# Kernel tuning notes

Measured on AMD Instinct MI355X. Metric: run time of the kernel, lower is better.

The kernel has to match this reference:

```python
import jax, jax.numpy as jnp
import numpy as np
import math

B, NX, NY = 4, 64, 64
IN_DIM, OUT_DIM = 3, 3
DIM, DEPTH, HEADS, DH, FF_MULT = 192, 6, 8, 64, 4
INNER = HEADS * DH              # 512
FF = DIM * FF_MULT              # 768
M = int(DH * math.log(DH))      # 266 random features (performer default)
GROUPS = 8
LATENT_STEPS = 1
EPS_SN, EPS_K, EPS_GN = 1e-5, 1e-4, 1e-5


def setup_inputs() -> dict:
    rng = np.random.default_rng(0)
    f = lambda *s: jnp.asarray(rng.standard_normal(s).astype(np.float32) * 0.02)
    # unitary forward operator (SVD-whitened in torch == orthogonal matrix)
    Q, _ = np.linalg.qr(rng.standard_normal((DIM, DIM)).astype(np.float32))
    return {
        "x": jnp.asarray(rng.standard_normal((B, NX, NY, IN_DIM)).astype(np.float32)),
        "to_in_w": f(DIM, IN_DIM), "to_in_b": f(DIM),
        "pos_emb": f(1, NX * NY, DIM),
        "proj": jnp.asarray(rng.standard_normal((DEPTH, M, DH)).astype(np.float32)),
        "sn_attn_g": jnp.ones((DEPTH,), jnp.float32),
        "wq": f(DEPTH, INNER, DIM), "wk": f(DEPTH, INNER, DIM), "wv": f(DEPTH, INNER, DIM),
        "wo": f(DEPTH, DIM, INNER), "bo": f(DEPTH, DIM),
        "sn_ff_g": jnp.ones((DEPTH,), jnp.float32),
        "w1": f(DEPTH, FF, DIM), "b1": f(DEPTH, FF),
        "w2": f(DEPTH, DIM, FF), "b2": f(DEPTH, DIM),
        "expand_w": f(DIM, DIM),
        "fwd_w": jnp.asarray(Q.astype(np.float32)),
        "dec_lin_w": f(DIM, DIM), "dec_lin_b": f(DIM),
        "gn_g": jnp.ones((DIM,), jnp.float32), "gn_b": jnp.zeros((DIM,), jnp.float32),
        "c9_w": f(DIM, DIM // GROUPS, 9, 9), "c9_b": f(DIM),
        "c7_w": f(DIM // 2, DIM // GROUPS, 7, 7), "c7_b": f(DIM // 2),
        "c5_w": f(DIM // 4, (DIM // 2) // GROUPS, 5, 5), "c5_b": f(DIM // 4),
        "c1_w": f(OUT_DIM, DIM // 4, 1, 1), "c1_b": f(OUT_DIM),
        "latent_steps": LATENT_STEPS,
    }


def _scalenorm(x, g):
    n = jnp.linalg.norm(x, axis=-1, keepdims=True) * (x.shape[-1] ** -0.5)
    return x / jnp.maximum(n, EPS_SN) * g


def _softmax_features(data, proj, is_query):
    # data: [b,h,n,d]; proj: [m,d] -> FAVOR+ softmax-kernel features [b,h,n,m]
    dn = data.shape[-1] ** -0.25
    ratio = proj.shape[0] ** -0.5
    dd = jnp.einsum('bhnd,md->bhnm', data * dn, proj)
    diag = 0.5 * jnp.sum(data * data, -1) * (dn * dn)  # [b,h,n]
    if is_query:
        mx = jnp.max(dd, axis=-1, keepdims=True)
    else:
        mx = jnp.max(dd, axis=(-1, -2), keepdims=True)
    return ratio * (jnp.exp(dd - diag[..., None] - mx) + EPS_K)


def _attn(x, proj, wq, wk, wv, wo, bo):
    b, n, _ = x.shape
    split = lambda t: t.reshape(b, n, HEADS, DH).transpose(0, 2, 1, 3)
    q = split(x @ wq.T); k = split(x @ wk.T); v = split(x @ wv.T)
    qp = _softmax_features(q, proj, True)
    kp = _softmax_features(k, proj, False)
    context = jnp.einsum('bhnm,bhnd->bhmd', kp, v)            # [b,h,m,d]
    denom = jnp.einsum('bhnm,bhm->bhn', qp, kp.sum(2))
    out = jnp.einsum('bhnm,bhmd->bhnd', qp, context) / denom[..., None]
    out = out.transpose(0, 2, 1, 3).reshape(b, n, INNER)
    return out @ wo.T + bo


def _circ_conv(x, w, b, groups):
    p = w.shape[-1] // 2
    x = jnp.pad(x, ((0, 0), (0, 0), (p, p), (p, p)), mode='wrap')
    y = jax.lax.conv_general_dilated(x, w, (1, 1), 'VALID',
        dimension_numbers=('NCHW', 'OIHW', 'NCHW'), feature_group_count=groups)
    return y + b[None, :, None, None]


def _group_norm(x, g, b):
    B_, C, H, W = x.shape
    xg = x.reshape(B_, GROUPS, C // GROUPS, H, W)
    mu = xg.mean((2, 3, 4), keepdims=True)
    var = xg.var((2, 3, 4), keepdims=True)
    xn = ((xg - mu) * jax.lax.rsqrt(var + EPS_GN)).reshape(B_, C, H, W)
    return xn * g[None, :, None, None] + b[None, :, None, None]


def reference(x, to_in_w, to_in_b, pos_emb, proj, sn_attn_g, wq, wk, wv, wo, bo,
              sn_ff_g, w1, b1, w2, b2, expand_w, fwd_w, dec_lin_w, dec_lin_b,
              gn_g, gn_b, c9_w, c9_b, c7_w, c7_b, c5_w, c5_b, c1_w, c1_b, latent_steps):
    b, nx, ny, _ = x.shape
    h = x @ to_in_w.T + to_in_b                       # [b,nx,ny,dim]
    h = h.reshape(b, nx * ny, DIM) + pos_emb[:, :nx * ny]
    for i in range(DEPTH):                             # Performer: prenorm attn + prenorm FF
        h = h + _attn(_scalenorm(h, sn_attn_g[i]), proj[i], wq[i], wk[i], wv[i], wo[i], bo[i])
        hn = _scalenorm(h, sn_ff_g[i])
        h = h + (jax.nn.gelu(hn @ w1[i].T + b1[i], approximate=False) @ w2[i].T + b2[i])
    h = h.reshape(b, nx, ny, DIM) @ expand_w.T        # expand_latent (no bias)
    u, us = h, []
    for _ in range(latent_steps):
        u = u @ fwd_w.T                               # unitary forward operator
        us.append(u)
    u = jnp.concatenate(us, 0)                        # [(b*t), nx, ny, c]
    y = u @ dec_lin_w.T + dec_lin_b
    y = y.transpose(0, 3, 1, 2)                       # NCHW
    y = _group_norm(y, gn_g, gn_b)
    y = jax.nn.gelu(_circ_conv(y, c9_w, c9_b, GROUPS), approximate=False)
    y = jax.nn.gelu(_circ_conv(y, c7_w, c7_b, GROUPS), approximate=False)
    y = jax.nn.gelu(_circ_conv(y, c5_w, c5_b, GROUPS), approximate=False)
    y = jax.lax.conv_general_dilated(y, c1_w, (1, 1), 'VALID',
        dimension_numbers=('NCHW', 'OIHW', 'NCHW')) + c1_b[None, :, None, None]
    # einops '(b t) c nx ny -> b t nx ny c'
    y = y.reshape(b, latent_steps, OUT_DIM, nx, ny).transpose(0, 1, 3, 4, 2)
    return y
```

## Files before the change

kernel.cpp:

```cpp
#include <hip/hip_runtime.h>
#include <cmath>

#define NB      4
#define NTOK    4096
#define BNTOK   16384
#define CDIM    192
#define CINNER  512
#define NHEADS  8
#define DHEAD   64
#define CFF     768
#define MFEAT   266
#define NDEPTH  6

#define DN      0.35355339059327373f
#define RATIO   0.06131393394849658f

typedef unsigned short u16;
typedef __attribute__((ext_vector_type(8))) short s16x8;
typedef __attribute__((ext_vector_type(8))) u16  u16x8;
typedef __attribute__((ext_vector_type(4))) float f32x4;

#define OFF_H    0ull
#define OFF_HN   3145728ull
#define OFF_Q    6291456ull
#define OFF_K    14680064ull
#define OFF_V    23068672ull
#define OFF_BIG  31457280ull
#define OFF_PJ   44040192ull
#define OFF_CTXT 44163072ull
#define OFF_KMAX 47368192ull
#define OFF_GNP  47368448ull
#define OFF_GNS  47369472ull
#define OFF_WHI  47370240ull
#define OFF_WLO  49489920ull
#define WOFF_QKV 0ull
#define WOFF_WO  1769472ull
#define WOFF_W1  2359296ull
#define WOFF_W2  3244032ull
#define WOFF_EXP 4128768ull
#define WOFF_FWD 4165632ull
#define WOFF_DEC 4202496ull

#define PJL      20480
#define NSEG     16
#define CTXP     20800

__device__ __forceinline__ float gelu_f(float x) {
    return 0.5f * x * (1.0f + erff(x * 0.7071067811865476f));
}
__device__ __forceinline__ unsigned f2ord(float f) {
    int i = __float_as_int(f);
    return (i >= 0) ? ((unsigned)i | 0x80000000u) : (unsigned)(~i);
}
__device__ __forceinline__ float ord2f(unsigned u) {
    int i = (u & 0x80000000u) ? (int)(u & 0x7fffffffu) : ~(int)u;
    return __int_as_float(i);
}
__device__ __forceinline__ void split_bf16(float a, u16& h, u16& l) {
    unsigned ua = __float_as_uint(a);
    unsigned rh = (ua + 0x7FFFu + ((ua >> 16) & 1u)) >> 16;
    h = (u16)rh;
    float hf = __uint_as_float(rh << 16);
    float lo = a - hf;
    unsigned ul = __float_as_uint(lo);
    unsigned rl = (ul + 0x7FFFu + ((ul >> 16) & 1u)) >> 16;
    l = (u16)rl;
}
__device__ __forceinline__ u16 hi_bf16(float a) {
    unsigned ua = __float_as_uint(a);
    return (u16)((ua + 0x7FFFu + ((ua >> 16) & 1u)) >> 16);
}

__global__ __launch_bounds__(256) void cvt_qkv(const float* __restrict__ wq,
    const float* __restrict__ wk, const float* __restrict__ wv,
    u16* __restrict__ hi, u16* __restrict__ lo)
{
    int idx = blockIdx.x * 256 + threadIdx.x;
    int l = idx / 294912, rem = idx - l * 294912;
    int r = rem / 192, c = rem - r * 192;
    float v;
    if (r < 512)       v = wq[((size_t)l * 512 + r) * 192 + c];
    else if (r < 1024) v = wk[((size_t)l * 512 + (r - 512)) * 192 + c];
    else               v = wv[((size_t)l * 512 + (r - 1024)) * 192 + c];
    u16 h, lw; split_bf16(v, h, lw);
    hi[idx] = h; lo[idx] = lw;
}

__global__ __launch_bounds__(256) void cvt_w(const float* __restrict__ src,
    u16* __restrict__ hi, u16* __restrict__ lo, int n)
{
    int idx = blockIdx.x * 256 + threadIdx.x;
    if (idx < n) {
        u16 h, l; split_bf16(src[idx], h, l);
        hi[idx] = h; lo[idx] = l;
    }
}

__global__ __launch_bounds__(256) void cvt_dec(const float* __restrict__ e,
    const float* __restrict__ f, const float* __restrict__ d,
    u16* __restrict__ hi, u16* __restrict__ lo)
{
    int idx = blockIdx.x * 256 + threadIdx.x;
    if (idx >= 110592) return;
    int which = idx / 36864, rem = idx - which * 36864;
    float v = (which == 0) ? e[rem] : (which == 1) ? f[rem] : d[rem];
    u16 h, l; split_bf16(v, h, l);
    hi[idx] = h; lo[idx] = l;
}

__global__ __launch_bounds__(256) void cvt_pj(const float* __restrict__ proj,
    u16* __restrict__ hi, u16* __restrict__ lo)
{
    int idx = blockIdx.x * 256 + threadIdx.x;
    int l = idx / PJL, rem = idx - l * PJL;
    int m = rem >> 6, k = rem & 63;
    float v = (m < MFEAT) ? proj[(size_t)l * MFEAT * DHEAD + m * 64 + k] : 0.f;
    u16 h, lw; split_bf16(v, h, lw);
    hi[idx] = h; lo[idx] = lw;
}

__global__ __launch_bounds__(256) void input_embed(const float* __restrict__ x,
    const float* __restrict__ w, const float* __restrict__ bvec,
    const float* __restrict__ pos, float* __restrict__ h)
{
    int idx = blockIdx.x * 256 + threadIdx.x;
    int row = idx / CDIM, c = idx - row * CDIM;
    int p = row & (NTOK - 1);
    const float* xr = x + (size_t)row * 3;
    h[idx] = xr[0]*w[c*3+0] + xr[1]*w[c*3+1] + xr[2]*w[c*3+2] + bvec[c] + pos[(size_t)p*CDIM + c];
}

__global__ __launch_bounds__(256) void rownorm_kernel(const float* __restrict__ in,
    float* __restrict__ sv, const float* __restrict__ gptr, int gidx)
{
    int wv = threadIdx.x >> 6, lane = threadIdx.x & 63;
    int row = blockIdx.x * 4 + wv;
    const float* p = in + (size_t)row * CDIM;
    float x0 = p[lane], x1 = p[lane + 64], x2 = p[lane + 128];
    float ss = x0*x0 + x1*x1 + x2*x2;
    #pragma unroll
    for (int off = 32; off; off >>= 1) ss += __shfl_xor(ss, off);
    if (lane == 0) {
        float g = gptr[gidx];
        float n = sqrtf(ss * (1.0f / 192.0f));
        sv[row] = g / fmaxf(n, 1e-5f);
    }
}

#define LP 40
__global__ __launch_bounds__(256) void gemm_mfma(const float* __restrict__ A,
    const float* __restrict__ ascale,
    const u16* __restrict__ Bhi, const u16* __restrict__ Blo,
    const float* __restrict__ bias, const float* __restrict__ resid,
    float* __restrict__ C, int M, int N, int K, int epi)
{
    __shared__ u16 a_hi[128 * LP], a_lo[128 * LP], b_hi[128 * LP], b_lo[128 * LP];
    const int tid = threadIdx.x;
    const int n0 = blockIdx.x * 128, m0 = blockIdx.y * 128;
    const int wave = tid >> 6, lane = tid & 63;
    const int wr = wave >> 1, wc = wave & 1;
    const int fr = lane & 15, q = lane >> 4;
    const bool wactive = (n0 + wc * 64) < N;
    f32x4 acc[4][4];
    #pragma unroll
    for (int i = 0; i < 4; ++i)
        #pragma unroll
        for (int j = 0; j < 4; ++j) { acc[i][j][0]=0.f; acc[i][j][1]=0.f; acc[i][j][2]=0.f; acc[i][j][3]=0.f; }

    const int srow = tid >> 1, sc0 = (tid & 1) * 16;
    const float* aptr = A + (size_t)(m0 + srow) * K + sc0;
    const float as = ascale ? ascale[m0 + srow] : 1.0f;
    const bool bval = (n0 + srow) < N;
    const u16* bhp = Bhi + (size_t)(n0 + srow) * K + sc0;
    const u16* blp = Blo + (size_t)(n0 + srow) * K + sc0;
    const int soff = srow * LP + sc0;
    const int aoffb = (wr * 64 + fr) * LP + q * 8;
    const int boffb = (wc * 64 + fr) * LP + q * 8;

    for (int kc = 0; kc < K; kc += 32) {
        float4 f0 = *(const float4*)(aptr + kc);
        float4 f1 = *(const float4*)(aptr + kc + 4);
        float4 f2 = *(const float4*)(aptr + kc + 8);
        float4 f3 = *(const float4*)(aptr + kc + 12);
        u16x8 h0, l0, h1, l1;
        {
            float v[16] = {f0.x,f0.y,f0.z,f0.w, f1.x,f1.y,f1.z,f1.w,
                           f2.x,f2.y,f2.z,f2.w, f3.x,f3.y,f3.z,f3.w};
            u16 hh[16], ll[16];
            #pragma unroll
            for (int i = 0; i < 16; ++i) { float sv = v[i] * as; split_bf16(sv, hh[i], ll[i]); }
            #pragma unroll
            for (int i = 0; i < 8; ++i) { h0[i]=hh[i]; l0[i]=ll[i]; h1[i]=hh[8+i]; l1[i]=ll[8+i]; }
        }
        *(u16x8*)&a_hi[soff]     = h0;  *(u16x8*)&a_hi[soff + 8] = h1;
        *(u16x8*)&a_lo[soff]     = l0;  *(u16x8*)&a_lo[soff + 8] = l1;
        u16x8 bh0 = (u16x8)0, bh1 = (u16x8)0, bl0 = (u16x8)0, bl1 = (u16x8)0;
        if (bval) {
            bh0 = *(const u16x8*)(bhp + kc);  bh1 = *(const u16x8*)(bhp + kc + 8);
            bl0 = *(const u16x8*)(blp + kc);  bl1 = *(const u16x8*)(blp + kc + 8);
        }
        *(u16x8*)&b_hi[soff]     = bh0;  *(u16x8*)&b_hi[soff + 8] = bh1;
        *(u16x8*)&b_lo[soff]     = bl0;  *(u16x8*)&b_lo[soff + 8] = bl1;
        __syncthreads();
        if (wactive) {
            s16x8 Ah[4], Al[4], Bh[4], Bl[4];
            #pragma unroll
            for (int t = 0; t < 4; ++t) {
                Ah[t] = *(const s16x8*)&a_hi[aoffb + t * 16 * LP];
                Al[t] = *(const s16x8*)&a_lo[aoffb + t * 16 * LP];
                Bh[t] = *(const s16x8*)&b_hi[boffb + t * 16 * LP];
                Bl[t] = *(const s16x8*)&b_lo[boffb + t * 16 * LP];
            }
            #pragma unroll
            for (int i = 0; i < 4; ++i)
                #pragma unroll
                for (int j = 0; j < 4; ++j)
                    acc[i][j] = __builtin_amdgcn_mfma_f32_16x16x32_bf16(Ah[i], Bh[j], acc[i][j], 0, 0, 0);
            #pragma unroll
            for (int i = 0; i < 4; ++i)
                #pragma unroll
                for (int j = 0; j < 4; ++j)
                    acc[i][j] = __builtin_amdgcn_mfma_f32_16x16x32_bf16(Ah[i], Bl[j], acc[i][j], 0, 0, 0);
            #pragma unroll
            for (int i = 0; i < 4; ++i)
                #pragma unroll
                for (int j = 0; j < 4; ++j)
                    acc[i][j] = __builtin_amdgcn_mfma_f32_16x16x32_bf16(Al[i], Bh[j], acc[i][j], 0, 0, 0);
        }
        __syncthreads();
    }
    const int c0 = n0 + wc * 64;
    const int rowb = m0 + wr * 64;
    #pragma unroll
    for (int j = 0; j < 4; ++j) {
        int c = c0 + j * 16 + fr;
        if (c >= N) continue;
        float bb = (epi & 1) ? bias[c] : 0.f;
        float* cp;
        if (epi & 8) cp = C + (size_t)(c >> 9) * 8388608ull + (size_t)(c & 511);
        else         cp = C + c;
        const float* rp = (epi & 4) ? (resid + c) : nullptr;
        #pragma unroll
        for (int i = 0; i < 4; ++i) {
            #pragma unroll
            for (int r = 0; r < 4; ++r) {
                int row = rowb + i * 16 + q * 4 + r;
                float val = acc[i][j][r] + bb;
                if (epi & 2) val = gelu_f(val);
                if (epi & 4) val += rp[(size_t)row * N];
                size_t off = (epi & 8) ? (size_t)row * 512 : (size_t)row * N;
                cp[off] = val;
            }
        }
    }
}

__global__ void kmax_init(unsigned* kmaxu) {
    if (threadIdx.x < NDEPTH * 32) kmaxu[threadIdx.x] = 0u;
}

__global__ __launch_bounds__(256) void kmax2_kernel(const float* __restrict__ Km,
    const u16* __restrict__ pjh, unsigned* __restrict__ kmaxu)
{
    __shared__ __align__(16) u16 khi[64 * 72];
    __shared__ float wred[4];
    const int tid = threadIdx.x;
    const int nt = blockIdx.x, bh = blockIdx.y;
    const int b = bh >> 3, hh = bh & 7;
    const int wave = tid >> 6, lane = tid & 63;
    const int fr = lane & 15, quad = lane >> 4;
    float lm = -1e30f;
    const size_t kbase = ((size_t)b * NTOK) * CINNER + hh * DHEAD;
    for (int ch = 0; ch < 4; ++ch) {
        const int n0 = nt * 256 + ch * 64;
        __syncthreads();
        {
            int tok = tid >> 2, koff = (tid & 3) * 16;
            const float* kp = Km + kbase + (size_t)(n0 + tok) * CINNER + koff;
            u16 hh16[16];
            #pragma unroll
            for (int qd = 0; qd < 4; ++qd) {
                float4 f = *(const float4*)(kp + qd * 4);
                hh16[qd*4+0] = hi_bf16(f.x * DN); hh16[qd*4+1] = hi_bf16(f.y * DN);
                hh16[qd*4+2] = hi_bf16(f.z * DN); hh16[qd*4+3] = hi_bf16(f.w * DN);
            }
            u16x8 v0, v1;
            #pragma unroll
            for (int i = 0; i < 8; ++i) { v0[i] = hh16[i]; v1[i] = hh16[8+i]; }
            *(u16x8*)&khi[tok * 72 + koff] = v0;
            *(u16x8*)&khi[tok * 72 + koff + 8] = v1;
        }
        __syncthreads();
        int rowA = (wave * 16 + fr) * 72;
        s16x8 A0 = *(const s16x8*)&khi[rowA + quad * 8];
        s16x8 A1 = *(const s16x8*)&khi[rowA + 32 + quad * 8];
        for (int ct = 0; ct < 17; ++ct) {
            const u16* bp = pjh + (ct * 16 + fr) * 64 + quad * 8;
            s16x8 B0 = *(const s16x8*)bp;
            s16x8 B1 = *(const s16x8*)(bp + 32);
            f32x4 t; t[0]=0.f; t[1]=0.f; t[2]=0.f; t[3]=0.f;
            t = __builtin_amdgcn_mfma_f32_16x16x32_bf16(A0, B0, t, 0, 0, 0);
            t = __builtin_amdgcn_mfma_f32_16x16x32_bf16(A1, B1, t, 0, 0, 0);
            if (ct * 16 + fr < MFEAT) {
                #pragma unroll
                for (int r = 0; r < 4; ++r) lm = fmaxf(lm, t[r]);
            }
        }
    }
    #pragma unroll
    for (int off = 32; off; off >>= 1) lm = fmaxf(lm, __shfl_xor(lm, off));
    if (lane == 0) wred[wave] = lm;
    __syncthreads();
    if (tid == 0) {
        float m = fmaxf(fmaxf(wred[0], wred[1]), fmaxf(wred[2], wred[3]));
        atomicMax(kmaxu + bh, f2ord(m));
    }
}

__global__ __launch_bounds__(256) void ctx2_kernel(const float* __restrict__ Km,
    const float* __restrict__ Vm, const u16* __restrict__ pjh, const u16* __restrict__ pjl,
    const unsigned* __restrict__ kmaxu, float* __restrict__ part)
{
    __shared__ __align__(16) u16 khi[32 * 72], klo[32 * 72];
    __shared__ __align__(16) u16 vth[80 * 40], vtl[80 * 40];
    __shared__ __align__(16) u16 kph[4][16 * 40], kpl[4][16 * 40];
    __shared__ float diag[32];
    const int tid = threadIdx.x;
    const int bh = blockIdx.x, seg = blockIdx.y;
    const int b = bh >> 3, hh = bh & 7;
    const int wave = tid >> 6, lane = tid & 63;
    const int fr = lane & 15, quad = lane >> 4;
    const float kmx = ord2f(kmaxu[bh]);
    for (int i = tid; i < 16 * 40; i += 256) {
        int row = 64 + i / 40, col = i - (i / 40) * 40;
        vth[row * 40 + col] = (row == 64) ? (u16)0x3F80 : (u16)0;
        vtl[row * 40 + col] = 0;
    }
    f32x4 accv[5][5];
    #pragma unroll
    for (int i = 0; i < 5; ++i)
        #pragma unroll
        for (int j = 0; j < 5; ++j) { accv[i][j][0]=0.f; accv[i][j][1]=0.f; accv[i][j][2]=0.f; accv[i][j][3]=0.f; }
    const size_t rowbase = ((size_t)b * NTOK) * CINNER + hh * DHEAD;
    u16* sh = kph[wave];  u16* sl = kpl[wave];
    for (int nc = 0; nc < 8; ++nc) {
        const int n0 = seg * 256 + nc * 32;
        __syncthreads();
        {
            int tok = tid >> 3, koff = (tid & 7) * 8;
            const float* kp = Km + rowbase + (size_t)(n0 + tok) * CINNER + koff;
            float4 f0 = *(const float4*)kp;
            float4 f1 = *(const float4*)(kp + 4);
            float v[8] = {f0.x*DN, f0.y*DN, f0.z*DN, f0.w*DN, f1.x*DN, f1.y*DN, f1.z*DN, f1.w*DN};
            u16x8 hv, lv; float ps = 0.f;
            #pragma unroll
            for (int i = 0; i < 8; ++i) { u16 h, l; split_bf16(v[i], h, l); hv[i]=h; lv[i]=l; ps += v[i]*v[i]; }
            *(u16x8*)&khi[tok * 72 + koff] = hv;
            *(u16x8*)&klo[tok * 72 + koff] = lv;
            ps += __shfl_xor(ps, 1); ps += __shfl_xor(ps, 2); ps += __shfl_xor(ps, 4);
            if ((tid & 7) == 0) diag[tok] = 0.5f * ps;
            const float* vp = Vm + rowbase + (size_t)(n0 + tok) * CINNER + koff;
            float4 g0 = *(const float4*)vp;
            float4 g1 = *(const float4*)(vp + 4);
            float vv[8] = {g0.x, g0.y, g0.z, g0.w, g1.x, g1.y, g1.z, g1.w};
            #pragma unroll
            for (int i = 0; i < 8; ++i) {
                u16 h, l; split_bf16(vv[i], h, l);
                vth[(koff + i) * 40 + tok] = h;
                vtl[(koff + i) * 40 + tok] = l;
            }
        }
        __syncthreads();
        s16x8 Ah[2][2], Al[2][2];
        #pragma unroll
        for (int rt = 0; rt < 2; ++rt) {
            int rowA = (rt * 16 + fr) * 72;
            Ah[rt][0] = *(const s16x8*)&khi[rowA + quad * 8];
            Ah[rt][1] = *(const s16x8*)&khi[rowA + 32 + quad * 8];
            Al[rt][0] = *(const s16x8*)&klo[rowA + quad * 8];
            Al[rt][1] = *(const s16x8*)&klo[rowA + 32 + quad * 8];
        }
        for (int mc = 0; mc < 5; ++mc) {
            const int ct = mc * 4 + wave;
            const u16* bph = pjh + (ct * 16 + fr) * 64 + quad * 8;
            const u16* bpl = pjl + (ct * 16 + fr) * 64 + quad * 8;
            s16x8 B0h = *(const s16x8*)bph, B1h = *(const s16x8*)(bph + 32);
            s16x8 B0l = *(const s16x8*)bpl, B1l = *(const s16x8*)(bpl + 32);
            const bool valid = (ct * 16 + fr) < MFEAT;
            #pragma unroll
            for (int rt = 0; rt < 2; ++rt) {
                f32x4 dd; dd[0]=0.f; dd[1]=0.f; dd[2]=0.f; dd[3]=0.f;
                dd = __builtin_amdgcn_mfma_f32_16x16x32_bf16(Ah[rt][0], B0h, dd, 0, 0, 0);
                dd = __builtin_amdgcn_mfma_f32_16x16x32_bf16(Ah[rt][0], B0l, dd, 0, 0, 0);
                dd = __builtin_amdgcn_mfma_f32_16x16x32_bf16(Al[rt][0], B0h, dd, 0, 0, 0);
                dd = __builtin_amdgcn_mfma_f32_16x16x32_bf16(Ah[rt][1], B1h, dd, 0, 0, 0);
                dd = __builtin_amdgcn_mfma_f32_16x16x32_bf16(Ah[rt][1], B1l, dd, 0, 0, 0);
                dd = __builtin_amdgcn_mfma_f32_16x16x32_bf16(Al[rt][1], B1h, dd, 0, 0, 0);
                ushort4 ph, pl;
                #pragma unroll
                for (int r = 0; r < 4; ++r) {
                    float dgv = diag[rt * 16 + quad * 4 + r];
                    float val = valid ? RATIO * (expf(dd[r] - dgv - kmx) + 1e-4f) : 0.f;
                    u16 h, l; split_bf16(val, h, l);
                    (&ph.x)[r] = h; (&pl.x)[r] = l;
                }
                *(ushort4*)&sh[fr * 40 + rt * 16 + quad * 4] = ph;
                *(ushort4*)&sl[fr * 40 + rt * 16 + quad * 4] = pl;
            }
            s16x8 Bh = *(const s16x8*)&sh[fr * 40 + quad * 8];
            s16x8 Bl = *(const s16x8*)&sl[fr * 40 + quad * 8];
            #pragma unroll
            for (int rt2 = 0; rt2 < 5; ++rt2) {
                s16x8 Vh = *(const s16x8*)&vth[(rt2 * 16 + fr) * 40 + quad * 8];
                s16x8 Vl = *(const s16x8*)&vtl[(rt2 * 16 + fr) * 40 + quad * 8];
                accv[rt2][mc] = __builtin_amdgcn_mfma_f32_16x16x32_bf16(Vh, Bh, accv[rt2][mc], 0, 0, 0);
                accv[rt2][mc] = __builtin_amdgcn_mfma_f32_16x16x32_bf16(Vh, Bl, accv[rt2][mc], 0, 0, 0);
                accv[rt2][mc] = __builtin_amdgcn_mfma_f32_16x16x32_bf16(Vl, Bh, accv[rt2][mc], 0, 0, 0);
            }
        }
    }
    float* pb = part + ((size_t)(seg * 32 + bh)) * CTXP;
    #pragma unroll
    for (int rt2 = 0; rt2 < 5; ++rt2) {
        #pragma unroll
        for (int mc = 0; mc < 5; ++mc) {
            int ct = mc * 4 + wave;
            #pragma unroll
            for (int r = 0; r < 4; ++r) {
                int row = rt2 * 16 + quad * 4 + r;
                if (row < 65)
                    pb[(size_t)row * 320 + ct * 16 + fr] = accv[rt2][mc][r];
            }
        }
    }
}

__global__ __launch_bounds__(256) void ctxt_reduce(const float* __restrict__ part,
    u16* __restrict__ cth, u16* __restrict__ ctl)
{
    int idx = blockIdx.x * 256 + threadIdx.x;
    if (idx >= 32 * CTXP) return;
    float s = 0.f;
    #pragma unroll
    for (int sg = 0; sg < NSEG; ++sg) s += part[(size_t)sg * 32 * CTXP + idx];
    int bh = idx / CTXP, rem = idx - bh * CTXP;
    int row = rem / 320, col = rem - row * 320;
    u16 h, l; split_bf16(s, h, l);
    size_t o = ((size_t)bh * 80 + row) * 320 + col;
    cth[o] = h; ctl[o] = l;
}

__global__ __launch_bounds__(256) void qside2_kernel(const float* __restrict__ Qm,
    const u16* __restrict__ pjh, const u16* __restrict__ pjl,
    const u16* __restrict__ cth, const u16* __restrict__ ctl,
    float* __restrict__ attn_out)
{
    __shared__ __align__(16) u16 qhi[64 * 72], qlo[64 * 72];
    __shared__ __align__(16) u16 slabh[4][16 * 72], slabl[4][16 * 72];
    __shared__ float diag[64];
    const int tid = threadIdx.x;
    const int nt = blockIdx.x, bh = blockIdx.y;
    const int b = bh >> 3, hh = bh & 7;
    const int wave = tid >> 6, lane = tid & 63;
    const int fr = lane & 15, quad = lane >> 4;
    const int n0 = nt * 64;
    {
        int tok = tid >> 2, koff = (tid & 3) * 16;
        const float* qp = Qm + ((size_t)(b * NTOK + n0 + tok)) * CINNER + hh * DHEAD + koff;
        float v[16]; float ps = 0.f;
        #pragma unroll
        for (int qd = 0; qd < 4; ++qd) {
            float4 f = *(const float4*)(qp + qd * 4);
            v[qd*4+0]=f.x*DN; v[qd*4+1]=f.y*DN; v[qd*4+2]=f.z*DN; v[qd*4+3]=f.w*DN;
        }
        u16x8 h0, l0, h1, l1;
        #pragma unroll
        for (int i = 0; i < 8; ++i) {
            u16 h, l; split_bf16(v[i], h, l); h0[i]=h; l0[i]=l;
            split_bf16(v[8+i], h, l); h1[i]=h; l1[i]=l;
        }
        #pragma unroll
        for (int i = 0; i < 16; ++i) ps += v[i]*v[i];
        *(u16x8*)&qhi[tok * 72 + koff] = h0;  *(u16x8*)&qhi[tok * 72 + koff + 8] = h1;
        *(u16x8*)&qlo[tok * 72 + koff] = l0;  *(u16x8*)&qlo[tok * 72 + koff + 8] = l1;
        ps += __shfl_xor(ps, 1); ps += __shfl_xor(ps, 2);
        if ((tid & 3) == 0) diag[tok] = 0.5f * ps;
    }
    __syncthreads();
    f32x4 dd[20];
    #pragma unroll
    for (int ct = 0; ct < 20; ++ct) { dd[ct][0]=0.f; dd[ct][1]=0.f; dd[ct][2]=0.f; dd[ct][3]=0.f; }
    {
        int rowA = (wave * 16 + fr) * 72;
        s16x8 A0h = *(const s16x8*)&qhi[rowA + quad * 8];
        s16x8 A1h = *(const s16x8*)&qhi[rowA + 32 + quad * 8];
        s16x8 A0l = *(const s16x8*)&qlo[rowA + quad * 8];
        s16x8 A1l = *(const s16x8*)&qlo[rowA + 32 + quad * 8];
        #pragma unroll
        for (int ct = 0; ct < 20; ++ct) {
            const u16* bph = pjh + (ct * 16 + fr) * 64 + quad * 8;
            const u16* bpl = pjl + (ct * 16 + fr) * 64 + quad * 8;
            s16x8 B0h = *(const s16x8*)bph, B1h = *(const s16x8*)(bph + 32);
            s16x8 B0l = *(const s16x8*)bpl, B1l = *(const s16x8*)(bpl + 32);
            dd[ct] = __builtin_amdgcn_mfma_f32_16x16x32_bf16(A0h, B0h, dd[ct], 0, 0, 0);
            dd[ct] = __builtin_amdgcn_mfma_f32_16x16x32_bf16(A0h, B0l, dd[ct], 0, 0, 0);
            dd[ct] = __builtin_amdgcn_mfma_f32_16x16x32_bf16(A0l, B0h, dd[ct], 0, 0, 0);
            dd[ct] = __builtin_amdgcn_mfma_f32_16x16x32_bf16(A1h, B1h, dd[ct], 0, 0, 0);
            dd[ct] = __builtin_amdgcn_mfma_f32_16x16x32_bf16(A1h, B1l, dd[ct], 0, 0, 0);
            dd[ct] = __builtin_amdgcn_mfma_f32_16x16x32_bf16(A1l, B1h, dd[ct], 0, 0, 0);
        }
    }
    float pm[4] = {-1e30f, -1e30f, -1e30f, -1e30f};
    #pragma unroll
    for (int ct = 0; ct < 20; ++ct) {
        if (ct * 16 + fr < MFEAT) {
            #pragma unroll
            for (int r = 0; r < 4; ++r) pm[r] = fmaxf(pm[r], dd[ct][r]);
        }
    }
    #pragma unroll
    for (int r = 0; r < 4; ++r) {
        pm[r] = fmaxf(pm[r], __shfl_xor(pm[r], 1));
        pm[r] = fmaxf(pm[r], __shfl_xor(pm[r], 2));
        pm[r] = fmaxf(pm[r], __shfl_xor(pm[r], 4));
        pm[r] = fmaxf(pm[r], __shfl_xor(pm[r], 8));
    }
    float dg[4];
    #pragma unroll
    for (int r = 0; r < 4; ++r) dg[r] = diag[wave * 16 + quad * 4 + r];
    #pragma unroll
    for (int ct = 0; ct < 20; ++ct) {
        bool valid = (ct * 16 + fr) < MFEAT;
        #pragma unroll
        for (int r = 0; r < 4; ++r)
            dd[ct][r] = valid ? RATIO * (expf(dd[ct][r] - dg[r] - pm[r]) + 1e-4f) : 0.f;
    }
    f32x4 acc[5];
    #pragma unroll
    for (int dt = 0; dt < 5; ++dt) { acc[dt][0]=0.f; acc[dt][1]=0.f; acc[dt][2]=0.f; acc[dt][3]=0.f; }
    u16* sh = slabh[wave];  u16* sl = slabl[wave];
    for (int mc = 0; mc < 5; ++mc) {
        #pragma unroll
        for (int c = 0; c < 4; ++c) {
            int ct = mc * 4 + c;
            #pragma unroll
            for (int r = 0; r < 4; ++r) {
                u16 h, l; split_bf16(dd[ct][r], h, l);
                int tok = quad * 4 + r;
                sh[tok * 72 + c * 16 + fr] = h;
                sl[tok * 72 + c * 16 + fr] = l;
            }
        }
        #pragma unroll
        for (int ks = 0; ks < 2; ++ks) {
            s16x8 Ah = *(const s16x8*)&sh[fr * 72 + ks * 32 + quad * 8];
            s16x8 Al = *(const s16x8*)&sl[fr * 72 + ks * 32 + quad * 8];
            #pragma unroll
            for (int dt = 0; dt < 5; ++dt) {
                const u16* bph = cth + ((size_t)bh * 80 + dt * 16 + fr) * 320 + mc * 64 + ks * 32 + quad * 8;
                const u16* bpl = ctl + ((size_t)bh * 80 + dt * 16 + fr) * 320 + mc * 64 + ks * 32 + quad * 8;
                s16x8 Bh = *(const s16x8*)bph;
                s16x8 Bl = *(const s16x8*)bpl;
                acc[dt] = __builtin_amdgcn_mfma_f32_16x16x32_bf16(Ah, Bh, acc[dt], 0, 0, 0);
                acc[dt] = __builtin_amdgcn_mfma_f32_16x16x32_bf16(Ah, Bl, acc[dt], 0, 0, 0);
                acc[dt] = __builtin_amdgcn_mfma_f32_16x16x32_bf16(Al, Bh, acc[dt], 0, 0, 0);
            }
        }
    }
    #pragma unroll
    for (int r = 0; r < 4; ++r) {
        float denom = __shfl(acc[4][r], lane & 48);
        float inv = 1.0f / denom;
        int token = n0 + wave * 16 + quad * 4 + r;
        float* op = attn_out + ((size_t)(b * NTOK + token)) * CINNER + hh * DHEAD;
        #pragma unroll
        for (int dt = 0; dt < 4; ++dt)
            op[dt * 16 + fr] = acc[dt][r] * inv;
    }
}

__global__ __launch_bounds__(256) void gn_part_kernel(const float* __restrict__ y,
    float2* __restrict__ part)
{
    __shared__ float s_s[256], s_q[256];
    const int tid = threadIdx.x;
    const int sp = blockIdx.x, g = blockIdx.y, b = blockIdx.z;
    int p = sp * 256 + tid;
    const float* base = y + ((size_t)(b * NTOK + p)) * CDIM + g * 24;
    float s = 0.f, q = 0.f;
    #pragma unroll
    for (int i = 0; i < 24; ++i) { float v = base[i]; s += v; q += v * v; }
    s_s[tid] = s; s_q[tid] = q;
    __syncthreads();
    for (int st = 128; st; st >>= 1) {
        if (tid < st) { s_s[tid] += s_s[tid + st]; s_q[tid] += s_q[tid + st]; }
        __syncthreads();
    }
    if (tid == 0) part[(b * 8 + g) * 16 + sp] = make_float2(s_s[0], s_q[0]);
}

__global__ void gn_stat_kernel(const float2* __restrict__ part, float2* __restrict__ stat)
{
    int bg = threadIdx.x;
    if (bg < 32) {
        float s = 0.f, q = 0.f;
        for (int i = 0; i < 16; ++i) { float2 v = part[bg * 16 + i]; s += v.x; q += v.y; }
        float mean = s * (1.0f / 98304.0f);
        float var = q * (1.0f / 98304.0f) - mean * mean;
        stat[bg] = make_float2(mean, rsqrtf(var + 1e-5f));
    }
}

__global__ __launch_bounds__(256) void gn_apply_kernel(const float* __restrict__ y,
    const float2* __restrict__ stat, const float* __restrict__ gg,
    const float* __restrict__ gb, float* __restrict__ out)
{
    __shared__ float tile[64][65];
    const int tid = threadIdx.x;
    const int pt = blockIdx.x, ct = blockIdx.y, b = blockIdx.z;
    const int p0 = pt * 64, c0 = ct * 64;
    #pragma unroll
    for (int r = 0; r < 4; ++r) {
        int id = tid + r * 256;
        int pr = id >> 4, kq = (id & 15) * 4;
        float4 v = *(const float4*)(y + ((size_t)(b * NTOK + p0 + pr)) * CDIM + c0 + kq);
        tile[pr][kq+0] = v.x; tile[pr][kq+1] = v.y; tile[pr][kq+2] = v.z; tile[pr][kq+3] = v.w;
    }
    __syncthreads();
    const int cc = tid >> 6, pp = tid & 63;
    #pragma unroll
    for (int i = 0; i < 16; ++i) {
        int c = c0 + cc * 16 + i;
        int g = c / 24;
        float2 st = stat[b * 8 + g];
        float v = tile[pp][cc * 16 + i];
        out[((size_t)(b * CDIM + c)) * NTOK + p0 + pp] = (v - st.x) * st.y * gg[c] + gb[c];
    }
}

template<int KS, int CIN, int COUT, int OX, int YS, int OCB>
__global__ __launch_bounds__(256) void circ_conv4(const float* __restrict__ in,
    const float* __restrict__ w, const float* __restrict__ bias,
    float* __restrict__ out, int do_gelu)
{
    constexpr int P   = KS / 2;
    constexpr int ICG = CIN / 8;
    constexpr int OCG = COUT / 8;
    constexpr int TW  = 64 + 2 * P;
    constexpr int TR  = 64 / YS + 2 * P;
    constexpr int RS0 = (TW + 3) & ~3;
    constexpr int RS  = (RS0 % 8 == 0) ? RS0 + 4 : RS0;
    constexpr int TCX = 64 / OX;
    constexpr int RV  = (OX + KS - 1 + 3) & ~3;
    constexpr int NLD = (TR * TW + 255) / 256;
    __shared__ __align__(16) float tile[2][TR * RS];
    const int tid = threadIdx.x;
    const int oc0 = blockIdx.x * OCB;
    const int y0  = blockIdx.y * (64 / YS);
    const int b   = blockIdx.z;
    const int g   = oc0 / OCG;
    const int tx  = tid % TCX, ty = tid / TCX;
    int srcs[NLD], dsts[NLD];
    #pragma unroll
    for (int j = 0; j < NLD; ++j) {
        int idx = tid + j * 256;
        if (idx < TR * TW) {
            int r = idx / TW, c = idx - r * TW;
            int gy = (y0 + r - P) & 63, gx = (c - P) & 63;
            srcs[j] = gy * 64 + gx;
            dsts[j] = r * RS + c;
        } else { srcs[j] = 0; dsts[j] = -1; }
    }
    float acc[OCB][OX] = {};
    const float* ip0 = in + ((size_t)(b * CIN + g * ICG)) * 4096;
    #pragma unroll 1
    for (int ic = 0; ic < ICG; ic += 2) {
        __syncthreads();
        const float* ipa = ip0 + (size_t)ic * 4096;
        const float* ipb = ipa + 4096;
        #pragma unroll
        for (int j = 0; j < NLD; ++j)
            if (dsts[j] >= 0) {
                tile[0][dsts[j]] = ipa[srcs[j]];
                tile[1][dsts[j]] = ipb[srcs[j]];
            }
        __syncthreads();
        #pragma unroll 1
        for (int pp = 0; pp < 2; ++pp) {
            const float* wp = w + ((size_t)oc0 * ICG + ic + pp) * (KS * KS);
            const float* tp = tile[pp];
            #pragma unroll 1
            for (int ky = 0; ky < KS; ++ky) {
                float wreg[OCB][KS];
                #pragma unroll
                for (int oc = 0; oc < OCB; ++oc)
                    #pragma unroll
                    for (int kx = 0; kx < KS; ++kx)
                        wreg[oc][kx] = wp[(size_t)oc * ICG * KS * KS + ky * KS + kx];
                float rv[RV];
                const float* rp = &tp[(ty + ky) * RS + tx * OX];
                #pragma unroll
                for (int q2 = 0; q2 < RV / 4; ++q2)
                    *(float4*)&rv[q2 * 4] = *(const float4*)(rp + q2 * 4);
                #pragma unroll
                for (int kx = 0; kx < KS; ++kx)
                    #pragma unroll
                    for (int oc = 0; oc < OCB; ++oc)
                        #pragma unroll
                        for (int ox = 0; ox < OX; ++ox)
                            acc[oc][ox] += rv[kx + ox] * wreg[oc][kx];
            }
        }
    }
    const int y = y0 + ty, x = tx * OX;
    #pragma unroll
    for (int oc = 0; oc < OCB; ++oc) {
        float bv = bias[oc0 + oc];
        float vo[OX];
        #pragma unroll
        for (int ox = 0; ox < OX; ++ox) {
            float vv = acc[oc][ox] + bv;
            vo[ox] = do_gelu ? gelu_f(vv) : vv;
        }
        float* op = out + (((size_t)(b * COUT + oc0 + oc) * 64 + y)) * 64 + x;
        #pragma unroll
        for (int q2 = 0; q2 < OX / 4; ++q2)
            *(float4*)(op + q2 * 4) = *(float4*)&vo[q2 * 4];
    }
}

__global__ __launch_bounds__(256) void conv1_kernel(const float* __restrict__ in,
    const float* __restrict__ w, const float* __restrict__ bias, float* __restrict__ out)
{
    int idx = blockIdx.x * 256 + threadIdx.x;
    int b = idx >> 12, p = idx & 4095;
    float a0 = bias[0], a1 = bias[1], a2 = bias[2];
    const float* ip = in + (size_t)b * 48 * NTOK + p;
    #pragma unroll 8
    for (int ic = 0; ic < 48; ++ic) {
        float v = ip[(size_t)ic * NTOK];
        a0 += v * w[ic]; a1 += v * w[48 + ic]; a2 += v * w[96 + ic];
    }
    float* op = out + (size_t)idx * 3;
    op[0] = a0; op[1] = a1; op[2] = a2;
}

static inline void gemm_mf(hipStream_t s, const float* A, const float* ascale,
                           const u16* Bhi, const u16* Blo,
                           const float* bias, const float* resid, float* C,
                           int M, int N, int K, int epi)
{
    dim3 g((N + 127) / 128, M / 128);
    hipLaunchKernelGGL(gemm_mfma, g, dim3(256), 0, s, A, ascale, Bhi, Blo, bias, resid, C, M, N, K, epi);
}

extern "C" void kernel_launch(void* const* d_in, const int* in_sizes, int n_in,
                              void* d_out, int out_size, void* d_ws, size_t ws_size,
                              hipStream_t stream)
{
    (void)in_sizes; (void)n_in; (void)out_size; (void)ws_size;
    const float* x        = (const float*)d_in[0];
    const float* to_in_w  = (const float*)d_in[1];
    const float* to_in_b  = (const float*)d_in[2];
    const float* pos_emb  = (const float*)d_in[3];
    const float* proj     = (const float*)d_in[4];
    const float* sn_attn_g= (const float*)d_in[5];
    const float* wq       = (const float*)d_in[6];
    const float* wk       = (const float*)d_in[7];
    const float* wv       = (const float*)d_in[8];
    const float* wo       = (const float*)d_in[9];
    const float* bo       = (const float*)d_in[10];
    const float* sn_ff_g  = (const float*)d_in[11];
    const float* w1       = (const float*)d_in[12];
    const float* b1       = (const float*)d_in[13];
    const float* w2       = (const float*)d_in[14];
    const float* b2       = (const float*)d_in[15];
    const float* expand_w = (const float*)d_in[16];
    const float* fwd_w    = (const float*)d_in[17];
    const float* dec_lin_w= (const float*)d_in[18];
    const float* dec_lin_b= (const float*)d_in[19];
    const float* gn_g     = (const float*)d_in[20];
    const float* gn_b     = (const float*)d_in[21];
    const float* c9_w     = (const float*)d_in[22];
    const float* c9_b     = (const float*)d_in[23];
    const float* c7_w     = (const float*)d_in[24];
    const float* c7_b     = (const float*)d_in[25];
    const float* c5_w     = (const float*)d_in[26];
    const float* c5_b     = (const float*)d_in[27];
    const float* c1_w     = (const float*)d_in[28];
    const float* c1_b     = (const float*)d_in[29];
    float* out = (float*)d_out;

    float* ws = (float*)d_ws;
    float* h   = ws + OFF_H;
    float* hn  = ws + OFF_HN;
    float* sbuf = ws + OFF_HN;
    float* q   = ws + OFF_Q;
    float* k   = ws + OFF_K;
    float* v   = ws + OFF_V;
    float* big = ws + OFF_BIG;
    u16* pjhi = (u16*)(ws + OFF_PJ);
    u16* pjlo = pjhi + 6 * PJL;
    u16* cthi = (u16*)(ws + OFF_CTXT);
    u16* ctlo = cthi + 32 * 80 * 320;
    unsigned* kmaxu = (unsigned*)(ws + OFF_KMAX);
    float2* gnp = (float2*)(ws + OFF_GNP);
    float2* gns = (float2*)(ws + OFF_GNS);
    u16* whi = (u16*)(ws + OFF_WHI);
    u16* wlo = (u16*)(ws + OFF_WLO);

    hipLaunchKernelGGL(input_embed, dim3(BNTOK * CDIM / 256), dim3(256), 0, stream,
                       x, to_in_w, to_in_b, pos_emb, h);
    hipLaunchKernelGGL(kmax_init, dim3(1), dim3(256), 0, stream, kmaxu);
    hipLaunchKernelGGL(cvt_qkv, dim3(6912), dim3(256), 0, stream, wq, wk, wv,
                       whi + WOFF_QKV, wlo + WOFF_QKV);
    hipLaunchKernelGGL(cvt_w, dim3(2304), dim3(256), 0, stream, wo, whi + WOFF_WO, wlo + WOFF_WO, 589824);
    hipLaunchKernelGGL(cvt_w, dim3(3456), dim3(256), 0, stream, w1, whi + WOFF_W1, wlo + WOFF_W1, 884736);
    hipLaunchKernelGGL(cvt_w, dim3(3456), dim3(256), 0, stream, w2, whi + WOFF_W2, wlo + WOFF_W2, 884736);
    hipLaunchKernelGGL(cvt_dec, dim3(432), dim3(256), 0, stream, expand_w, fwd_w, dec_lin_w,
                       whi + WOFF_EXP, wlo + WOFF_EXP);
    hipLaunchKernelGGL(cvt_pj, dim3(480), dim3(256), 0, stream, proj, pjhi, pjlo);

    for (int l = 0; l < NDEPTH; ++l) {
        const float* bo_l = bo + (size_t)l * CDIM;
        const float* b1_l = b1 + (size_t)l * CFF;
        const float* b2_l = b2 + (size_t)l * CDIM;
        const u16* pjh_l = pjhi + (size_t)l * PJL;
        const u16* pjl_l = pjlo + (size_t)l * PJL;
        unsigned* kmax_l = kmaxu + l * 32;

        hipLaunchKernelGGL(rownorm_kernel, dim3(BNTOK / 4), dim3(256), 0, stream, h, sbuf, sn_attn_g, l);
        gemm_mf(stream, h, sbuf, whi + WOFF_QKV + (size_t)l * 294912, wlo + WOFF_QKV + (size_t)l * 294912,
                nullptr, nullptr, q, BNTOK, 1536, CDIM, 8 | 16);
        hipLaunchKernelGGL(kmax2_kernel, dim3(16, 32), dim3(256), 0, stream, k, pjh_l, kmax_l);
        hipLaunchKernelGGL(ctx2_kernel, dim3(32, NSEG), dim3(256), 0, stream, k, v, pjh_l, pjl_l, kmax_l, big);
        hipLaunchKernelGGL(ctxt_reduce, dim3((32 * CTXP + 255) / 256), dim3(256), 0, stream, big, cthi, ctlo);
        hipLaunchKernelGGL(qside2_kernel, dim3(64, 32), dim3(256), 0, stream, q, pjh_l, pjl_l, cthi, ctlo, k);
        gemm_mf(stream, k, nullptr, whi + WOFF_WO + (size_t)l * 98304, wlo + WOFF_WO + (size_t)l * 98304,
                bo_l, h, h, BNTOK, CDIM, CINNER, 1 | 4);

        hipLaunchKernelGGL(rownorm_kernel, dim3(BNTOK / 4), dim3(256), 0, stream, h, sbuf, sn_ff_g, l);
        gemm_mf(stream, h, sbuf, whi + WOFF_W1 + (size_t)l * 147456, wlo + WOFF_W1 + (size_t)l * 147456,
                b1_l, nullptr, big, BNTOK, CFF, CDIM, 1 | 2 | 16);
        gemm_mf(stream, big, nullptr, whi + WOFF_W2 + (size_t)l * 147456, wlo + WOFF_W2 + (size_t)l * 147456,
                b2_l, h, h, BNTOK, CDIM, CFF, 1 | 4);
    }

    gemm_mf(stream, h, nullptr, whi + WOFF_EXP, wlo + WOFF_EXP, nullptr, nullptr, hn, BNTOK, CDIM, CDIM, 0);
    gemm_mf(stream, hn, nullptr, whi + WOFF_FWD, wlo + WOFF_FWD, nullptr, nullptr, h, BNTOK, CDIM, CDIM, 0);
    gemm_mf(stream, h, nullptr, whi + WOFF_DEC, wlo + WOFF_DEC, dec_lin_b, nullptr, hn, BNTOK, CDIM, CDIM, 1);

    float* y0 = big;
    float* y1 = big + 3145728;
    float* y2 = big + 6291456;
    float* y3 = big + 7864320;
    hipLaunchKernelGGL(gn_part_kernel, dim3(16, 8, 4), dim3(256), 0, stream, hn, gnp);
    hipLaunchKernelGGL(gn_stat_kernel, dim3(1), dim3(32), 0, stream, gnp, gns);
    hipLaunchKernelGGL(gn_apply_kernel, dim3(64, 3, 4), dim3(256), 0, stream, hn, gns, gn_g, gn_b, y0);

    hipLaunchKernelGGL((circ_conv4<9, 192, 192, 8, 2, 2>), dim3(96, 2, 4), dim3(256), 0, stream,
                       y0, c9_w, c9_b, y1, 1);
    hipLaunchKernelGGL((circ_conv4<7, 192, 96, 8, 2, 2>), dim3(48, 2, 4), dim3(256), 0, stream,
                       y1, c7_w, c7_b, y2, 1);
    hipLaunchKernelGGL((circ_conv4<5, 96, 48, 4, 4, 2>), dim3(24, 4, 4), dim3(256), 0, stream,
                       y2, c5_w, c5_b, y3, 1);
    hipLaunchKernelGGL(conv1_kernel, dim3(BNTOK / 256), dim3(256), 0, stream, y3, c1_w, c1_b, out);
}
```

Baseline: 3.574 ms.

## Split-K the Wo and W2 GEMMs and fuse residual, bias and rownorm into combine

The narrow N=192 GEMMs for Wo and W2 now run with split-K over two segments, writing partial sums that a new combine kernel adds together with the bias and residual. The same pass computes each row's sum of squares for the next ScaleNorm, so the standalone rownorm launch per sublayer is gone. The GEMM derives the ScaleNorm scale from that sum of squares itself. This doubles the grid (2x128 tiles instead of 2x128 with one column wasted) for better CU occupancy, at the cost of extra partial-buffer traffic.

```diff
diff --git a/kernel.cpp b/kernel.cpp
--- a/kernel.cpp
+++ b/kernel.cpp
@@ -28,6 +28,7 @@
 #define OFF_BIG  31457280ull
 #define OFF_PJ   44040192ull
 #define OFF_CTXT 44163072ull
+#define OFF_SSQ  44982272ull
 #define OFF_KMAX 47368192ull
 #define OFF_GNP  47368448ull
 #define OFF_GNS  47369472ull
@@ -45,6 +46,13 @@
 #define NSEG     16
 #define CTXP     20800
 
+#define EP_BIAS  1
+#define EP_GELU  2
+#define EP_RESID 4
+#define EP_QKV   8
+#define EP_SROW  16
+#define EP_PART  32
+
 __device__ __forceinline__ float gelu_f(float x) {
     return 0.5f * x * (1.0f + erff(x * 0.7071067811865476f));
 }
@@ -131,7 +139,7 @@
 }
 
 __global__ __launch_bounds__(256) void rownorm_kernel(const float* __restrict__ in,
-    float* __restrict__ sv, const float* __restrict__ gptr, int gidx)
+    float* __restrict__ ssq)
 {
     int wv = threadIdx.x >> 6, lane = threadIdx.x & 63;
     int row = blockIdx.x * 4 + wv;
@@ -140,23 +148,48 @@
     float ss = x0*x0 + x1*x1 + x2*x2;
     #pragma unroll
     for (int off = 32; off; off >>= 1) ss += __shfl_xor(ss, off);
-    if (lane == 0) {
-        float g = gptr[gidx];
-        float n = sqrtf(ss * (1.0f / 192.0f));
-        sv[row] = g / fmaxf(n, 1e-5f);
-    }
+    if (lane == 0) ssq[row] = ss;
+}
+
+__global__ __launch_bounds__(256) void combine_kernel(const float* __restrict__ p0,
+    const float* __restrict__ p1, const float* __restrict__ bias,
+    float* __restrict__ h, float* __restrict__ ssq)
+{
+    int row = blockIdx.x * 16 + (threadIdx.x >> 4);
+    int lane16 = threadIdx.x & 15;
+    size_t base = (size_t)row * CDIM + lane16 * 12;
+    float s = 0.f;
+    #pragma unroll
+    for (int q2 = 0; q2 < 3; ++q2) {
+        float4 a = *(const float4*)(p0 + base + q2 * 4);
+        float4 b = *(const float4*)(p1 + base + q2 * 4);
+        float4 hv = *(const float4*)(h + base + q2 * 4);
+        float4 bb = *(const float4*)(bias + lane16 * 12 + q2 * 4);
+        float4 o;
+        o.x = a.x + b.x + hv.x + bb.x;
+        o.y = a.y + b.y + hv.y + bb.y;
+        o.z = a.z + b.z + hv.z + bb.z;
+        o.w = a.w + b.w + hv.w + bb.w;
+        *(float4*)(h + base + q2 * 4) = o;
+        s += o.x*o.x + o.y*o.y + o.z*o.z + o.w*o.w;
+    }
+    s += __shfl_xor(s, 1); s += __shfl_xor(s, 2);
+    s += __shfl_xor(s, 4); s += __shfl_xor(s, 8);
+    if (lane16 == 0) ssq[row] = s;
 }
 
 #define LP 40
 __global__ __launch_bounds__(256) void gemm_mfma(const float* __restrict__ A,
-    const float* __restrict__ ascale,
+    const float* __restrict__ ssq, const float* __restrict__ gptr, int gidx,
     const u16* __restrict__ Bhi, const u16* __restrict__ Blo,
     const float* __restrict__ bias, const float* __restrict__ resid,
-    float* __restrict__ C, int M, int N, int K, int epi)
+    float* __restrict__ C, float* __restrict__ C2,
+    int M, int N, int K, int Kstride, int epi)
 {
     __shared__ u16 a_hi[128 * LP], a_lo[128 * LP], b_hi[128 * LP], b_lo[128 * LP];
     const int tid = threadIdx.x;
     const int n0 = blockIdx.x * 128, m0 = blockIdx.y * 128;
+    const int kseg = blockIdx.z;
     const int wave = tid >> 6, lane = tid & 63;
     const int wr = wave >> 1, wc = wave & 1;
     const int fr = lane & 15, q = lane >> 4;
@@ -168,11 +201,16 @@
         for (int j = 0; j < 4; ++j) { acc[i][j][0]=0.f; acc[i][j][1]=0.f; acc[i][j][2]=0.f; acc[i][j][3]=0.f; }
 
     const int srow = tid >> 1, sc0 = (tid & 1) * 16;
-    const float* aptr = A + (size_t)(m0 + srow) * K + sc0;
-    const float as = ascale ? ascale[m0 + srow] : 1.0f;
+    const float* aptr = A + (size_t)(m0 + srow) * Kstride + (size_t)kseg * K + sc0;
+    float as = 1.0f;
+    if (epi & EP_SROW) {
+        float ssv = ssq[m0 + srow];
+        float nn = sqrtf(ssv * (1.0f / 192.0f));
+        as = gptr[gidx] / fmaxf(nn, 1e-5f);
+    }
     const bool bval = (n0 + srow) < N;
-    const u16* bhp = Bhi + (size_t)(n0 + srow) * K + sc0;
-    const u16* blp = Blo + (size_t)(n0 + srow) * K + sc0;
+    const u16* bhp = Bhi + (size_t)(n0 + srow) * Kstride + (size_t)kseg * K + sc0;
+    const u16* blp = Blo + (size_t)(n0 + srow) * Kstride + (size_t)kseg * K + sc0;
     const int soff = srow * LP + sc0;
     const int aoffb = (wr * 64 + fr) * LP + q * 8;
     const int boffb = (wc * 64 + fr) * LP + q * 8;
@@ -231,24 +269,40 @@
     }
     const int c0 = n0 + wc * 64;
     const int rowb = m0 + wr * 64;
+    if (epi & EP_PART) {
+        float* base = kseg ? C2 : C;
+        #pragma unroll
+        for (int j = 0; j < 4; ++j) {
+            int c = c0 + j * 16 + fr;
+            if (c >= N) continue;
+            #pragma unroll
+            for (int i = 0; i < 4; ++i)
+                #pragma unroll
+                for (int r = 0; r < 4; ++r) {
+                    int row = rowb + i * 16 + q * 4 + r;
+                    base[(size_t)row * N + c] = acc[i][j][r];
+                }
+        }
+        return;
+    }
     #pragma unroll
     for (int j = 0; j < 4; ++j) {
         int c = c0 + j * 16 + fr;
         if (c >= N) continue;
-        float bb = (epi & 1) ? bias[c] : 0.f;
+        float bb = (epi & EP_BIAS) ? bias[c] : 0.f;
         float* cp;
-        if (epi & 8) cp = C + (size_t)(c >> 9) * 8388608ull + (size_t)(c & 511);
-        else         cp = C + c;
-        const float* rp = (epi & 4) ? (resid + c) : nullptr;
+        if (epi & EP_QKV) cp = C + (size_t)(c >> 9) * 8388608ull + (size_t)(c & 511);
+        else              cp = C + c;
+        const float* rp = (epi & EP_RESID) ? (resid + c) : nullptr;
         #pragma unroll
         for (int i = 0; i < 4; ++i) {
             #pragma unroll
             for (int r = 0; r < 4; ++r) {
                 int row = rowb + i * 16 + q * 4 + r;
                 float val = acc[i][j][r] + bb;
-                if (epi & 2) val = gelu_f(val);
-                if (epi & 4) val += rp[(size_t)row * N];
-                size_t off = (epi & 8) ? (size_t)row * 512 : (size_t)row * N;
+                if (epi & EP_GELU) val = gelu_f(val);
+                if (epi & EP_RESID) val += rp[(size_t)row * N];
+                size_t off = (epi & EP_QKV) ? (size_t)row * 512 : (size_t)row * N;
                 cp[off] = val;
             }
         }
@@ -745,13 +799,16 @@
     op[0] = a0; op[1] = a1; op[2] = a2;
 }
 
-static inline void gemm_mf(hipStream_t s, const float* A, const float* ascale,
+static inline void gemm_mf(hipStream_t s, const float* A, const float* ssq,
+                           const float* gptr, int gidx,
                            const u16* Bhi, const u16* Blo,
-                           const float* bias, const float* resid, float* C,
-                           int M, int N, int K, int epi)
-{
-    dim3 g((N + 127) / 128, M / 128);
-    hipLaunchKernelGGL(gemm_mfma, g, dim3(256), 0, s, A, ascale, Bhi, Blo, bias, resid, C, M, N, K, epi);
+                           const float* bias, const float* resid,
+                           float* C, float* C2,
+                           int M, int N, int K, int Kstride, int epi, int kz)
+{
+    dim3 g((N + 127) / 128, M / 128, kz);
+    hipLaunchKernelGGL(gemm_mfma, g, dim3(256), 0, s, A, ssq, gptr, gidx, Bhi, Blo,
+                       bias, resid, C, C2, M, N, K, Kstride, epi);
 }
 
 extern "C" void kernel_launch(void* const* d_in, const int* in_sizes, int n_in,
@@ -794,7 +851,6 @@
     float* ws = (float*)d_ws;
     float* h   = ws + OFF_H;
     float* hn  = ws + OFF_HN;
-    float* sbuf = ws + OFF_HN;
     float* q   = ws + OFF_Q;
     float* k   = ws + OFF_K;
     float* v   = ws + OFF_V;
@@ -803,6 +859,7 @@
     u16* pjlo = pjhi + 6 * PJL;
     u16* cthi = (u16*)(ws + OFF_CTXT);
     u16* ctlo = cthi + 32 * 80 * 320;
+    float* ssq = ws + OFF_SSQ;
     unsigned* kmaxu = (unsigned*)(ws + OFF_KMAX);
     float2* gnp = (float2*)(ws + OFF_GNP);
     float2* gns = (float2*)(ws + OFF_GNS);
@@ -820,6 +877,7 @@
     hipLaunchKernelGGL(cvt_dec, dim3(432), dim3(256), 0, stream, expand_w, fwd_w, dec_lin_w,
                        whi + WOFF_EXP, wlo + WOFF_EXP);
     hipLaunchKernelGGL(cvt_pj, dim3(480), dim3(256), 0, stream, proj, pjhi, pjlo);
+    hipLaunchKernelGGL(rownorm_kernel, dim3(BNTOK / 4), dim3(256), 0, stream, h, ssq);
 
     for (int l = 0; l < NDEPTH; ++l) {
         const float* bo_l = bo + (size_t)l * CDIM;
@@ -829,26 +887,35 @@
         const u16* pjl_l = pjlo + (size_t)l * PJL;
         unsigned* kmax_l = kmaxu + l * 32;
 
-        hipLaunchKernelGGL(rownorm_kernel, dim3(BNTOK / 4), dim3(256), 0, stream, h, sbuf, sn_attn_g, l);
-        gemm_mf(stream, h, sbuf, whi + WOFF_QKV + (size_t)l * 294912, wlo + WOFF_QKV + (size_t)l * 294912,
-                nullptr, nullptr, q, BNTOK, 1536, CDIM, 8 | 16);
+        gemm_mf(stream, h, ssq, sn_attn_g, l,
+                whi + WOFF_QKV + (size_t)l * 294912, wlo + WOFF_QKV + (size_t)l * 294912,
+                nullptr, nullptr, q, nullptr, BNTOK, 1536, CDIM, CDIM, EP_QKV | EP_SROW, 1);
         hipLaunchKernelGGL(kmax2_kernel, dim3(16, 32), dim3(256), 0, stream, k, pjh_l, kmax_l);
         hipLaunchKernelGGL(ctx2_kernel, dim3(32, NSEG), dim3(256), 0, stream, k, v, pjh_l, pjl_l, kmax_l, big);
         hipLaunchKernelGGL(ctxt_reduce, dim3((32 * CTXP + 255) / 256), dim3(256), 0, stream, big, cthi, ctlo);
         hipLaunchKernelGGL(qside2_kernel, dim3(64, 32), dim3(256), 0, stream, q, pjh_l, pjl_l, cthi, ctlo, k);
-        gemm_mf(stream, k, nullptr, whi + WOFF_WO + (size_t)l * 98304, wlo + WOFF_WO + (size_t)l * 98304,
-                bo_l, h, h, BNTOK, CDIM, CINNER, 1 | 4);
-
-        hipLaunchKernelGGL(rownorm_kernel, dim3(BNTOK / 4), dim3(256), 0, stream, h, sbuf, sn_ff_g, l);
-        gemm_mf(stream, h, sbuf, whi + WOFF_W1 + (size_t)l * 147456, wlo + WOFF_W1 + (size_t)l * 147456,
-                b1_l, nullptr, big, BNTOK, CFF, CDIM, 1 | 2 | 16);
-        gemm_mf(stream, big, nullptr, whi + WOFF_W2 + (size_t)l * 147456, wlo + WOFF_W2 + (size_t)l * 147456,
-                b2_l, h, h, BNTOK, CDIM, CFF, 1 | 4);
-    }
-
-    gemm_mf(stream, h, nullptr, whi + WOFF_EXP, wlo + WOFF_EXP, nullptr, nullptr, hn, BNTOK, CDIM, CDIM, 0);
-    gemm_mf(stream, hn, nullptr, whi + WOFF_FWD, wlo + WOFF_FWD, nullptr, nullptr, h, BNTOK, CDIM, CDIM, 0);
-    gemm_mf(stream, h, nullptr, whi + WOFF_DEC, wlo + WOFF_DEC, dec_lin_b, nullptr, hn, BNTOK, CDIM, CDIM, 1);
+        gemm_mf(stream, k, nullptr, nullptr, 0,
+                whi + WOFF_WO + (size_t)l * 98304, wlo + WOFF_WO + (size_t)l * 98304,
+                nullptr, nullptr, big, big + 6291456, BNTOK, CDIM, CINNER / 2, CINNER, EP_PART, 2);
+        hipLaunchKernelGGL(combine_kernel, dim3(BNTOK / 16), dim3(256), 0, stream,
+                           big, big + 6291456, bo_l, h, ssq);
+
+        gemm_mf(stream, h, ssq, sn_ff_g, l,
+                whi + WOFF_W1 + (size_t)l * 147456, wlo + WOFF_W1 + (size_t)l * 147456,
+                b1_l, nullptr, big, nullptr, BNTOK, CFF, CDIM, CDIM, EP_BIAS | EP_GELU | EP_SROW, 1);
+        gemm_mf(stream, big, nullptr, nullptr, 0,
+                whi + WOFF_W2 + (size_t)l * 147456, wlo + WOFF_W2 + (size_t)l * 147456,
+                nullptr, nullptr, q, v, BNTOK, CDIM, CFF / 2, CFF, EP_PART, 2);
+        hipLaunchKernelGGL(combine_kernel, dim3(BNTOK / 16), dim3(256), 0, stream,
+                           q, v, b2_l, h, ssq);
+    }
+
+    gemm_mf(stream, h, nullptr, nullptr, 0, whi + WOFF_EXP, wlo + WOFF_EXP,
+            nullptr, nullptr, hn, nullptr, BNTOK, CDIM, CDIM, CDIM, 0, 1);
+    gemm_mf(stream, hn, nullptr, nullptr, 0, whi + WOFF_FWD, wlo + WOFF_FWD,
+            nullptr, nullptr, h, nullptr, BNTOK, CDIM, CDIM, CDIM, 0, 1);
+    gemm_mf(stream, h, nullptr, nullptr, 0, whi + WOFF_DEC, wlo + WOFF_DEC,
+            dec_lin_b, nullptr, hn, nullptr, BNTOK, CDIM, CDIM, CDIM, EP_BIAS, 1);
 
     float* y0 = big;
     float* y1 = big + 3145728;
```

Result: no change. 3.622 ms (+1.4%).
